# Optimization experiments

Hardware: AMD Instinct MI355X
Metric: run time of the kernel (lower is better)

The kernel has to match this reference:

```python
import jax, jax.numpy as jnp
import numpy as np

# Module config (from init_kwargs)
GRID_SHAPE = (128, 128, 128)
GRID_LOWER = jnp.array([0.0, 0.0, 0.0], jnp.float32)
GRID_STEPS = jnp.array([0.1, 0.1, 0.1], jnp.float32)
RADIUS = 0.2
R_CELLS = 2  # ceil(RADIUS / step): cells each side of a particle that can be within RADIUS
_o = np.arange(-R_CELLS, R_CELLS + 1)
OFFSETS = jnp.asarray(np.stack(np.meshgrid(_o, _o, _o, indexing='ij'), -1).reshape(-1, 3), jnp.int32)  # [K3,3]
GSHAPE_ARR = jnp.asarray(GRID_SHAPE, jnp.int32)
NCELLS = int(np.prod(GRID_SHAPE))


def _cubic_spline(d, h):
    # Standard 3D cubic-spline SPH kernel, support radius h.
    q = d / h
    sigma = 8.0 / (np.pi * h ** 3)
    w = jnp.where(q < 0.5, 1.0 - 6.0 * q ** 2 + 6.0 * q ** 3, 2.0 * (1.0 - q) ** 3)
    return sigma * jnp.where(q < 1.0, w, 0.0)


def _splat_one(locs, data, density):
    # locs [N,4] (xyz + inverse mass), data [N,C], density [N]
    pos, inv_mass = locs[:, :3], locs[:, 3]
    base = jnp.floor((pos - GRID_LOWER) / GRID_STEPS).astype(jnp.int32)          # [N,3] cell of particle
    cells = base[:, None, :] + OFFSETS[None, :, :]                                # [N,K3,3]
    centers = GRID_LOWER + (cells.astype(pos.dtype) + 0.5) * GRID_STEPS           # cell centers
    d = jnp.linalg.norm(centers - pos[:, None, :], axis=-1)                       # [N,K3]
    w = _cubic_spline(d, RADIUS)
    inb = jnp.all((cells >= 0) & (cells < GSHAPE_ARR), axis=-1)                   # [N,K3]
    # SPH interpolation weight: (m_j / rho_j) * W; locs w-component is INVERSE mass.
    coef = jnp.where(inb, w, 0.0) * (1.0 / (inv_mass * density))[:, None]         # [N,K3]
    vals = coef[..., None] * data[:, None, :]                                     # [N,K3,C]
    lin = (cells[..., 0] * GRID_SHAPE[1] + cells[..., 1]) * GRID_SHAPE[2] + cells[..., 2]
    lin = jnp.clip(lin, 0, NCELLS - 1)                                            # OOB coefs are zero
    C = data.shape[-1]
    grid = jnp.zeros((NCELLS, C), data.dtype)
    grid = grid.at[lin.reshape(-1)].add(vals.reshape(-1, C))
    return grid.reshape(GRID_SHAPE + (C,))


def setup_inputs() -> dict:
    key = jax.random.key(0)
    k1, k2, k3, k4 = jax.random.split(key, 4)
    B, N, C = 2, 100000, 4
    domain = jnp.asarray(GRID_SHAPE, jnp.float32) * GRID_STEPS  # [12.8]*3
    pos = jax.random.uniform(k1, (B, N, 3), jnp.float32) * domain + GRID_LOWER
    inv_mass = jax.random.uniform(k2, (B, N, 1), jnp.float32) * 0.9 + 0.1
    locs = jnp.concatenate([pos, inv_mass], axis=-1)
    data = jax.random.normal(k3, (B, N, C), jnp.float32)
    density = jax.random.uniform(k4, (B, N), jnp.float32) + 0.5
    return {"locs": locs, "data": data, "density": density}


def reference(locs, data, density):
    # -> [B, X, Y, Z, C]
    return jax.vmap(_splat_one)(locs, data, density)
```

## Files before the change

### kernel.cpp

```cpp
#include <hip/hip_runtime.h>


constexpr int GX = 128, GY = 128, GZ = 128;
constexpr int NC = GX * GY * GZ;
constexpr int BD = 64;
constexpr int NBIN = BD * BD * BD;
constexpr int NB_TOT = 2 * NBIN;
constexpr float STEP   = 0.1f;
constexpr float INV_H  = 5.0f;
constexpr float H2     = 0.04f;
constexpr float SIGMA  = 318.30988618379067f;

__global__ __launch_bounds__(256) void zero_kernel(float4* __restrict__ out, int n4) {
  int stride = gridDim.x * blockDim.x;
  for (int i = blockIdx.x * blockDim.x + threadIdx.x; i < n4; i += stride)
    out[i] = make_float4(0.f, 0.f, 0.f, 0.f);
}

__global__ __launch_bounds__(256) void splat_kernel(
    const float4* __restrict__ locs, const float4* __restrict__ data,
    const float* __restrict__ density, float* __restrict__ out,
    int nTotal, int nPart) {
  int pid = blockIdx.x * blockDim.x + threadIdx.x;
  if (pid >= nTotal) return;
  int ox = blockIdx.y;
  float4 loc = locs[pid];
  float scale = 1.0f / (loc.w * density[pid]);
  int bx = (int)floorf(loc.x / STEP);
  int by = (int)floorf(loc.y / STEP);
  int bz = (int)floorf(loc.z / STEP);
  int cx = bx + ox - 2;
  if ((unsigned)cx >= (unsigned)GX) return;
  float dx = ((float)cx + 0.5f) * STEP - loc.x;
  float dx2 = dx * dx;
  if (dx2 >= H2) return;
  float4 dat = data[pid];
  int b = (pid >= nPart) ? 1 : 0;
  float* outb = out + (size_t)b * NC * 4;
  for (int oy = 0; oy < 5; ++oy) {
    int cy = by + oy - 2;
    if ((unsigned)cy >= (unsigned)GY) continue;
    float dy = ((float)cy + 0.5f) * STEP - loc.y;
    float dxy2 = dx2 + dy * dy;
    if (dxy2 >= H2) continue;
    float* rowp = outb + (size_t)((cx * GY + cy) * GZ) * 4;
    for (int oz = 0; oz < 5; ++oz) {
      int cz = bz + oz - 2;
      if ((unsigned)cz >= (unsigned)GZ) continue;
      float dz = ((float)cz + 0.5f) * STEP - loc.z;
      float d2 = dxy2 + dz * dz;
      if (d2 >= H2) continue;
      float q = sqrtf(d2) * INV_H;
      float w = (q < 0.5f) ? (1.0f + 6.0f * q * q * (q - 1.0f))
                           : (2.0f * (1.0f - q) * (1.0f - q) * (1.0f - q));
      float coef = SIGMA * scale * w;
      float* cellp = rowp + cz * 4;
      unsafeAtomicAdd(cellp + 0, coef * dat.x);
      unsafeAtomicAdd(cellp + 1, coef * dat.y);
      unsafeAtomicAdd(cellp + 2, coef * dat.z);
      unsafeAtomicAdd(cellp + 3, coef * dat.w);
    }
  }
}


__device__ __forceinline__ int particle_bin(float4 l, int isB1) {
  int bx = (int)floorf(l.x / STEP);
  int by = (int)floorf(l.y / STEP);
  int bz = (int)floorf(l.z / STEP);
  bx = min(max(bx, 0), GX - 1) >> 1;
  by = min(max(by, 0), GY - 1) >> 1;
  bz = min(max(bz, 0), GZ - 1) >> 1;
  return (isB1 ? NBIN : 0) + ((bx * BD) + by) * BD + bz;
}

__global__ __launch_bounds__(256) void zero_counts(int4* __restrict__ c, int n4) {
  int stride = gridDim.x * blockDim.x;
  for (int i = blockIdx.x * blockDim.x + threadIdx.x; i < n4; i += stride)
    c[i] = make_int4(0, 0, 0, 0);
}

__global__ __launch_bounds__(256) void count_kernel(
    const float4* __restrict__ locs, int* __restrict__ counts,
    int nTotal, int nPart) {
  int pid = blockIdx.x * blockDim.x + threadIdx.x;
  if (pid >= nTotal) return;
  int bin = particle_bin(locs[pid], pid >= nPart);
  atomicAdd(counts + bin, 1);
}

__global__ __launch_bounds__(256) void scan1(
    const int* __restrict__ counts, int* __restrict__ starts,
    int* __restrict__ blockSums) {
  __shared__ int sh[256];
  int t = threadIdx.x, bid = blockIdx.x;
  int base = bid * 1024 + t * 4;
  int4 c = *reinterpret_cast<const int4*>(counts + base);
  int s = c.x + c.y + c.z + c.w;
  sh[t] = s;
  __syncthreads();
  for (int off = 1; off < 256; off <<= 1) {
    int x = (t >= off) ? sh[t - off] : 0;
    __syncthreads();
    sh[t] += x;
    __syncthreads();
  }
  int incl = sh[t];
  int run = incl - s;
  int4 o;
  o.x = run; run += c.x;
  o.y = run; run += c.y;
  o.z = run; run += c.z;
  o.w = run;
  *reinterpret_cast<int4*>(starts + base) = o;
  if (t == 255) blockSums[bid] = incl;
}

__global__ __launch_bounds__(256) void scan3(
    int* __restrict__ starts, const int* __restrict__ blockSums,
    int* __restrict__ cursor) {
  __shared__ int red[8];
  int t = threadIdx.x, bid = blockIdx.x;
  int part = ((t < bid) ? blockSums[t] : 0) +
             ((t + 256 < bid) ? blockSums[t + 256] : 0);
  for (int o = 32; o > 0; o >>= 1) part += __shfl_down(part, o);
  if ((t & 63) == 0) red[t >> 6] = part;
  __syncthreads();
  if (t == 0) red[0] = red[0] + red[1] + red[2] + red[3];
  __syncthreads();
  int off = red[0];
  int base = bid * 1024 + t * 4;
  int4 v = *reinterpret_cast<int4*>(starts + base);
  v.x += off; v.y += off; v.z += off; v.w += off;
  *reinterpret_cast<int4*>(starts + base) = v;
  *reinterpret_cast<int4*>(cursor + base) = v;
  if (bid == 511 && t == 0) starts[NB_TOT] = off + blockSums[511];
}

__global__ __launch_bounds__(256) void scatter_kernel(
    const float4* __restrict__ locs, const float4* __restrict__ data,
    const float* __restrict__ density, int* __restrict__ cursor,
    float4* __restrict__ sA, float4* __restrict__ sB,
    int nTotal, int nPart) {
  int pid = blockIdx.x * blockDim.x + threadIdx.x;
  if (pid >= nTotal) return;
  float4 l = locs[pid];
  float4 d = data[pid];
  float s = SIGMA / (l.w * density[pid]);
  int bin = particle_bin(l, pid >= nPart);
  int idx = atomicAdd(cursor + bin, 1);
  sA[idx] = make_float4(l.x, l.y, l.z, s * d.x);
  sB[idx] = make_float4(s * d.y, s * d.z, s * d.w, 0.f);
}

__global__ __launch_bounds__(256) void gather8_kernel(
    const int* __restrict__ starts, const float4* __restrict__ sA,
    const float4* __restrict__ sB, float4* __restrict__ out) {
  int tid = blockIdx.x * blockDim.x + threadIdx.x;
  int b   = tid >> 18;
  int blk = tid & ((1 << 18) - 1);
  int Bz = blk & 63;
  int By = (blk >> 6) & 63;
  int Bx = blk >> 12;

  int cx0 = 2 * Bx, cy0 = 2 * By, cz0 = 2 * Bz;
  float px0 = ((float)cx0 + 0.5f) * STEP;
  float px1 = ((float)(cx0 + 1) + 0.5f) * STEP;
  float py0 = ((float)cy0 + 0.5f) * STEP;
  float py1 = ((float)(cy0 + 1) + 0.5f) * STEP;
  float pz0 = ((float)cz0 + 0.5f) * STEP;
  float pz1 = ((float)(cz0 + 1) + 0.5f) * STEP;

  int lx = max(Bx - 1, 0), hx = min(Bx + 1, BD - 1);
  int ly = max(By - 1, 0), hy = min(By + 1, BD - 1);
  int lz = max(Bz - 1, 0), hz = min(Bz + 1, BD - 1);
  int bb = b ? NBIN : 0;

  float acc[2][2][2][4];
#pragma unroll
  for (int i = 0; i < 2; ++i)
#pragma unroll
    for (int j = 0; j < 2; ++j)
#pragma unroll
      for (int k = 0; k < 2; ++k)
#pragma unroll
        for (int c = 0; c < 4; ++c) acc[i][j][k][c] = 0.f;

  for (int ix = lx; ix <= hx; ++ix) {
    for (int iy = ly; iy <= hy; ++iy) {
      int base = bb + (((ix << 6) + iy) << 6);
      int s = starts[base + lz];
      int e = starts[base + hz + 1];
      for (int p = s; p < e; ++p) {
        float4 a = sA[p];
        float4 v = sB[p];
        float dx0 = a.x - px0, dx1 = a.x - px1;
        float dy0 = a.y - py0, dy1 = a.y - py1;
        float dz0 = a.z - pz0, dz1 = a.z - pz1;
        float dx2[2] = {dx0 * dx0, dx1 * dx1};
        float dy2[2] = {dy0 * dy0, dy1 * dy1};
        float dz2[2] = {dz0 * dz0, dz1 * dz1};
#pragma unroll
        for (int i = 0; i < 2; ++i) {
#pragma unroll
          for (int j = 0; j < 2; ++j) {
            float dxy = dx2[i] + dy2[j];
#pragma unroll
            for (int k = 0; k < 2; ++k) {
              float d2 = dxy + dz2[k];
              if (d2 < H2) {
                float q = sqrtf(d2) * INV_H;
                float om = 1.0f - q;
                float wh = 2.0f * om * om * om;
                float wl = fmaf(6.0f * q * q, q - 1.0f, 1.0f);
                float w = (q < 0.5f) ? wl : wh;
                acc[i][j][k][0] = fmaf(w, a.w, acc[i][j][k][0]);
                acc[i][j][k][1] = fmaf(w, v.x, acc[i][j][k][1]);
                acc[i][j][k][2] = fmaf(w, v.y, acc[i][j][k][2]);
                acc[i][j][k][3] = fmaf(w, v.z, acc[i][j][k][3]);
              }
            }
          }
        }
      }
    }
  }

#pragma unroll
  for (int i = 0; i < 2; ++i)
#pragma unroll
    for (int j = 0; j < 2; ++j)
#pragma unroll
      for (int k = 0; k < 2; ++k) {
        int cell = (((cx0 + i) * GY) + (cy0 + j)) * GZ + (cz0 + k);
        out[((size_t)b << 21) + cell] =
            make_float4(acc[i][j][k][0], acc[i][j][k][1],
                        acc[i][j][k][2], acc[i][j][k][3]);
      }
}

static inline size_t align_up(size_t x, size_t a) { return (x + a - 1) & ~(a - 1); }

extern "C" void kernel_launch(void* const* d_in, const int* in_sizes, int n_in,
                              void* d_out, int out_size, void* d_ws, size_t ws_size,
                              hipStream_t stream) {
  const float* locs    = (const float*)d_in[0];
  const float* data    = (const float*)d_in[1];
  const float* density = (const float*)d_in[2];
  float* out = (float*)d_out;

  int nTotal = in_sizes[2];
  int B      = out_size / (NC * 4);
  int nPart  = nTotal / B;

  size_t o_counts = 0;
  size_t o_starts = align_up(o_counts + sizeof(int) * NB_TOT, 256);
  size_t o_cursor = align_up(o_starts + sizeof(int) * (NB_TOT + 1), 256);
  size_t o_bsums  = align_up(o_cursor + sizeof(int) * NB_TOT, 256);
  size_t o_sA     = align_up(o_bsums + sizeof(int) * 513, 256);
  size_t o_sB     = align_up(o_sA + sizeof(float4) * (size_t)nTotal, 256);
  size_t need     = o_sB + sizeof(float4) * (size_t)nTotal;

  if (B != 2 || ws_size < need) {
    int n4 = out_size / 4;
    int zblocks = min((n4 + 255) / 256, 2048);
    zero_kernel<<<zblocks, 256, 0, stream>>>(reinterpret_cast<float4*>(out), n4);
    dim3 grid((nTotal + 255) / 256, 5);
    splat_kernel<<<grid, 256, 0, stream>>>(
        reinterpret_cast<const float4*>(locs),
        reinterpret_cast<const float4*>(data), density, out, nTotal, nPart);
    return;
  }

  char* ws = (char*)d_ws;
  int* counts   = (int*)(ws + o_counts);
  int* starts   = (int*)(ws + o_starts);
  int* cursor   = (int*)(ws + o_cursor);
  int* bsums    = (int*)(ws + o_bsums);
  float4* sA    = (float4*)(ws + o_sA);
  float4* sB    = (float4*)(ws + o_sB);

  int pblocks = (nTotal + 255) / 256;

  zero_counts<<<512, 256, 0, stream>>>((int4*)counts, NB_TOT / 4);
  count_kernel<<<pblocks, 256, 0, stream>>>(
      reinterpret_cast<const float4*>(locs), counts, nTotal, nPart);
  scan1<<<512, 256, 0, stream>>>(counts, starts, bsums);
  scan3<<<512, 256, 0, stream>>>(starts, bsums, cursor);
  scatter_kernel<<<pblocks, 256, 0, stream>>>(
      reinterpret_cast<const float4*>(locs),
      reinterpret_cast<const float4*>(data), density, cursor, sA, sB,
      nTotal, nPart);
  gather8_kernel<<<(2 * NBIN) / 256, 256, 0, stream>>>(
      starts, sA, sB, reinterpret_cast<float4*>(out));
}
```

Before: 176.9 us.

## Fuse scan via atomic chunk offsets and flatten gather loop across columns

Replaces the two-pass scan with a single kernel in which each chunk reserves its global offset through an atomic on a total cursor. Bins stay contiguous within a chunk but chunk order becomes arbitrary, so range ends are computed from starts plus counts. The gather kernel now walks all 9 neighbor columns in one flattened loop, which keeps lanes busy across uneven column lengths, and the per-cell weight branch becomes a select. It also switches to 128-thread blocks and replaces the zeroing kernel with a memset. The cost is that every lane now computes the full spline for all 8 cells per particle, including cells outside the radius.

```diff
diff --git a/kernel.cpp b/kernel.cpp
--- a/kernel.cpp
+++ b/kernel.cpp
@@ -74,12 +74,6 @@
   return (isB1 ? NBIN : 0) + ((bx * BD) + by) * BD + bz;
 }
 
-__global__ __launch_bounds__(256) void zero_counts(int4* __restrict__ c, int n4) {
-  int stride = gridDim.x * blockDim.x;
-  for (int i = blockIdx.x * blockDim.x + threadIdx.x; i < n4; i += stride)
-    c[i] = make_int4(0, 0, 0, 0);
-}
-
 __global__ __launch_bounds__(256) void count_kernel(
     const float4* __restrict__ locs, int* __restrict__ counts,
     int nTotal, int nPart) {
@@ -89,10 +83,11 @@
   atomicAdd(counts + bin, 1);
 }
 
-__global__ __launch_bounds__(256) void scan1(
+__global__ __launch_bounds__(256) void scan_fused(
     const int* __restrict__ counts, int* __restrict__ starts,
-    int* __restrict__ blockSums) {
+    int* __restrict__ cursor, int* __restrict__ totalCursor) {
   __shared__ int sh[256];
+  __shared__ int chunkBaseSh;
   int t = threadIdx.x, bid = blockIdx.x;
   int base = bid * 1024 + t * 4;
   int4 c = *reinterpret_cast<const int4*>(counts + base);
@@ -106,35 +101,16 @@
     __syncthreads();
   }
   int incl = sh[t];
-  int run = incl - s;
+  if (t == 255) chunkBaseSh = atomicAdd(totalCursor, incl);
+  __syncthreads();
+  int run = chunkBaseSh + incl - s;
   int4 o;
   o.x = run; run += c.x;
   o.y = run; run += c.y;
   o.z = run; run += c.z;
   o.w = run;
   *reinterpret_cast<int4*>(starts + base) = o;
-  if (t == 255) blockSums[bid] = incl;
-}
-
-__global__ __launch_bounds__(256) void scan3(
-    int* __restrict__ starts, const int* __restrict__ blockSums,
-    int* __restrict__ cursor) {
-  __shared__ int red[8];
-  int t = threadIdx.x, bid = blockIdx.x;
-  int part = ((t < bid) ? blockSums[t] : 0) +
-             ((t + 256 < bid) ? blockSums[t + 256] : 0);
-  for (int o = 32; o > 0; o >>= 1) part += __shfl_down(part, o);
-  if ((t & 63) == 0) red[t >> 6] = part;
-  __syncthreads();
-  if (t == 0) red[0] = red[0] + red[1] + red[2] + red[3];
-  __syncthreads();
-  int off = red[0];
-  int base = bid * 1024 + t * 4;
-  int4 v = *reinterpret_cast<int4*>(starts + base);
-  v.x += off; v.y += off; v.z += off; v.w += off;
-  *reinterpret_cast<int4*>(starts + base) = v;
-  *reinterpret_cast<int4*>(cursor + base) = v;
-  if (bid == 511 && t == 0) starts[NB_TOT] = off + blockSums[511];
+  *reinterpret_cast<int4*>(cursor + base) = o;
 }
 
 __global__ __launch_bounds__(256) void scatter_kernel(
@@ -153,9 +129,10 @@
   sB[idx] = make_float4(s * d.y, s * d.z, s * d.w, 0.f);
 }
 
-__global__ __launch_bounds__(256) void gather8_kernel(
-    const int* __restrict__ starts, const float4* __restrict__ sA,
-    const float4* __restrict__ sB, float4* __restrict__ out) {
+__global__ __launch_bounds__(128) void gather8f_kernel(
+    const int* __restrict__ starts, const int* __restrict__ counts,
+    const float4* __restrict__ sA, const float4* __restrict__ sB,
+    float4* __restrict__ out) {
   int tid = blockIdx.x * blockDim.x + threadIdx.x;
   int b   = tid >> 18;
   int blk = tid & ((1 << 18) - 1);
@@ -163,16 +140,11 @@
   int By = (blk >> 6) & 63;
   int Bx = blk >> 12;
 
-  int cx0 = 2 * Bx, cy0 = 2 * By, cz0 = 2 * Bz;
-  float px0 = ((float)cx0 + 0.5f) * STEP;
-  float px1 = ((float)(cx0 + 1) + 0.5f) * STEP;
-  float py0 = ((float)cy0 + 0.5f) * STEP;
-  float py1 = ((float)(cy0 + 1) + 0.5f) * STEP;
-  float pz0 = ((float)cz0 + 0.5f) * STEP;
-  float pz1 = ((float)(cz0 + 1) + 0.5f) * STEP;
-
-  int lx = max(Bx - 1, 0), hx = min(Bx + 1, BD - 1);
-  int ly = max(By - 1, 0), hy = min(By + 1, BD - 1);
+  int cx0 = Bx << 1, cy0 = By << 1, cz0 = Bz << 1;
+  float px0 = ((float)cx0 + 0.5f) * STEP, px1 = px0 + STEP;
+  float py0 = ((float)cy0 + 0.5f) * STEP, py1 = py0 + STEP;
+  float pz0 = ((float)cz0 + 0.5f) * STEP, pz1 = pz0 + STEP;
+
   int lz = max(Bz - 1, 0), hz = min(Bz + 1, BD - 1);
   int bb = b ? NBIN : 0;
 
@@ -186,40 +158,51 @@
 #pragma unroll
         for (int c = 0; c < 4; ++c) acc[i][j][k][c] = 0.f;
 
-  for (int ix = lx; ix <= hx; ++ix) {
-    for (int iy = ly; iy <= hy; ++iy) {
-      int base = bb + (((ix << 6) + iy) << 6);
-      int s = starts[base + lz];
-      int e = starts[base + hz + 1];
-      for (int p = s; p < e; ++p) {
-        float4 a = sA[p];
-        float4 v = sB[p];
-        float dx0 = a.x - px0, dx1 = a.x - px1;
-        float dy0 = a.y - py0, dy1 = a.y - py1;
-        float dz0 = a.z - pz0, dz1 = a.z - pz1;
-        float dx2[2] = {dx0 * dx0, dx1 * dx1};
-        float dy2[2] = {dy0 * dy0, dy1 * dy1};
-        float dz2[2] = {dz0 * dz0, dz1 * dz1};
-#pragma unroll
-        for (int i = 0; i < 2; ++i) {
-#pragma unroll
-          for (int j = 0; j < 2; ++j) {
-            float dxy = dx2[i] + dy2[j];
-#pragma unroll
-            for (int k = 0; k < 2; ++k) {
-              float d2 = dxy + dz2[k];
-              if (d2 < H2) {
-                float q = sqrtf(d2) * INV_H;
-                float om = 1.0f - q;
-                float wh = 2.0f * om * om * om;
-                float wl = fmaf(6.0f * q * q, q - 1.0f, 1.0f);
-                float w = (q < 0.5f) ? wl : wh;
-                acc[i][j][k][0] = fmaf(w, a.w, acc[i][j][k][0]);
-                acc[i][j][k][1] = fmaf(w, v.x, acc[i][j][k][1]);
-                acc[i][j][k][2] = fmaf(w, v.y, acc[i][j][k][2]);
-                acc[i][j][k][3] = fmaf(w, v.z, acc[i][j][k][3]);
-              }
-            }
+  int col = -1;
+  int p = 0, e = 0;
+  while (true) {
+    while (p >= e && col < 9) {
+      ++col;
+      if (col < 9) {
+        int ox = (col >= 6) ? 1 : ((col >= 3) ? 0 : -1);
+        int oy = col - ((ox + 1) * 3) - 1;
+        int ix = Bx + ox, iy = By + oy;
+        if (((unsigned)ix < (unsigned)BD) & ((unsigned)iy < (unsigned)BD)) {
+          int base = bb + (((ix << 6) + iy) << 6);
+          p = starts[base + lz];
+          e = starts[base + hz] + counts[base + hz];
+        }
+      }
+    }
+    if (__all(col >= 9)) break;
+    if (col < 9) {
+      float4 a = sA[p];
+      float4 v = sB[p];
+      ++p;
+      float dx0 = a.x - px0, dx1 = a.x - px1;
+      float dy0 = a.y - py0, dy1 = a.y - py1;
+      float dz0 = a.z - pz0, dz1 = a.z - pz1;
+      float dx2[2] = {dx0 * dx0, dx1 * dx1};
+      float dy2[2] = {dy0 * dy0, dy1 * dy1};
+      float dz2[2] = {dz0 * dz0, dz1 * dz1};
+#pragma unroll
+      for (int i = 0; i < 2; ++i) {
+#pragma unroll
+        for (int j = 0; j < 2; ++j) {
+          float dxy = dx2[i] + dy2[j];
+#pragma unroll
+          for (int k = 0; k < 2; ++k) {
+            float d2 = dxy + dz2[k];
+            float q = sqrtf(d2) * INV_H;
+            float om = 1.0f - q;
+            float wh = 2.0f * om * om * om;
+            float wl = fmaf(6.0f * q * q, q - 1.0f, 1.0f);
+            float w = (q < 0.5f) ? wl : wh;
+            w = (d2 < H2) ? w : 0.0f;
+            acc[i][j][k][0] = fmaf(w, a.w, acc[i][j][k][0]);
+            acc[i][j][k][1] = fmaf(w, v.x, acc[i][j][k][1]);
+            acc[i][j][k][2] = fmaf(w, v.y, acc[i][j][k][2]);
+            acc[i][j][k][3] = fmaf(w, v.z, acc[i][j][k][3]);
           }
         }
       }
@@ -254,10 +237,10 @@
   int nPart  = nTotal / B;
 
   size_t o_counts = 0;
-  size_t o_starts = align_up(o_counts + sizeof(int) * NB_TOT, 256);
-  size_t o_cursor = align_up(o_starts + sizeof(int) * (NB_TOT + 1), 256);
-  size_t o_bsums  = align_up(o_cursor + sizeof(int) * NB_TOT, 256);
-  size_t o_sA     = align_up(o_bsums + sizeof(int) * 513, 256);
+  size_t o_total  = sizeof(int) * NB_TOT;
+  size_t o_starts = align_up(o_total + sizeof(int), 256);
+  size_t o_cursor = align_up(o_starts + sizeof(int) * NB_TOT, 256);
+  size_t o_sA     = align_up(o_cursor + sizeof(int) * NB_TOT, 256);
   size_t o_sB     = align_up(o_sA + sizeof(float4) * (size_t)nTotal, 256);
   size_t need     = o_sB + sizeof(float4) * (size_t)nTotal;
 
@@ -274,23 +257,22 @@
 
   char* ws = (char*)d_ws;
   int* counts   = (int*)(ws + o_counts);
+  int* totalCur = (int*)(ws + o_total);
   int* starts   = (int*)(ws + o_starts);
   int* cursor   = (int*)(ws + o_cursor);
-  int* bsums    = (int*)(ws + o_bsums);
   float4* sA    = (float4*)(ws + o_sA);
   float4* sB    = (float4*)(ws + o_sB);
 
   int pblocks = (nTotal + 255) / 256;
 
-  zero_counts<<<512, 256, 0, stream>>>((int4*)counts, NB_TOT / 4);
+  hipMemsetAsync(ws, 0, sizeof(int) * (NB_TOT + 1), stream);
   count_kernel<<<pblocks, 256, 0, stream>>>(
       reinterpret_cast<const float4*>(locs), counts, nTotal, nPart);
-  scan1<<<512, 256, 0, stream>>>(counts, starts, bsums);
-  scan3<<<512, 256, 0, stream>>>(starts, bsums, cursor);
+  scan_fused<<<NB_TOT / 1024, 256, 0, stream>>>(counts, starts, cursor, totalCur);
   scatter_kernel<<<pblocks, 256, 0, stream>>>(
       reinterpret_cast<const float4*>(locs),
       reinterpret_cast<const float4*>(data), density, cursor, sA, sB,
       nTotal, nPart);
-  gather8_kernel<<<(2 * NBIN) / 256, 256, 0, stream>>>(
-      starts, sA, sB, reinterpret_cast<float4*>(out));
-}
+  gather8f_kernel<<<(2 * NBIN) / 128, 128, 0, stream>>>(
+      starts, counts, sA, sB, reinterpret_cast<float4*>(out));
+}
```

New measurement: 207.9 us. +17.6%, slower.
